# Optimization experiments

Measured on AMD Instinct MI355X. Metric: run time of the kernel, lower is better.

The kernel has to match this reference:

```python
import jax, jax.numpy as jnp
import numpy as np
import math

B, H, S, D = 2, 12, 2048, 64

def setup_inputs() -> dict:
    key = jax.random.key(0)
    kq, kk, kv, km = jax.random.split(key, 4)
    Q = jax.random.normal(kq, (B, H, S, D), dtype=jnp.float32)
    K = jax.random.normal(kk, (B, H, S, D), dtype=jnp.float32)
    V = jax.random.normal(kv, (B, H, S, D), dtype=jnp.float32)
    mask = jax.random.randint(km, (B, 1, S, S), 0, 2, dtype=jnp.int32)
    return {"Q": Q, "K": K, "V": V, "mask": mask}

def reference(Q, K, V, mask):
    d_k = K.shape[-1]
    # [B,H,S,S] scores
    scores = jnp.einsum('bhqd,bhkd->bhqk', Q, K) / math.sqrt(d_k)
    scores = jnp.where(mask == 0, jnp.float32(-1e20), scores)
    attn = jax.nn.softmax(scores, axis=-1)
    # dropout p=0 -> identity
    return jnp.einsum('bhqk,bhkd->bhqd', attn, V)
```

## Files before the change

kernel.cpp:

```cpp
#include <hip/hip_runtime.h>
#include <hip/hip_bf16.h>
#include <math.h>


#define BB 2
#define HH 12
#define SS 2048
#define DD 64
#define BQ 128
#define BK 64
#define GG 4
#define KG (SS / GG)
#define NTG (KG / BK)
#define LT 76
#define NROWS (BB * HH * SS)
#define QSCALE 0.1803368801111f

typedef __attribute__((ext_vector_type(8))) short bf8_t;
typedef __attribute__((ext_vector_type(4))) short bf4_t;
typedef __attribute__((ext_vector_type(4))) float f4_t;
typedef __attribute__((ext_vector_type(4))) unsigned u4_t;
typedef unsigned long long u64;

__device__ __forceinline__ short f2bf(float f) {
    __hip_bfloat16 h = __float2bfloat16(f);
    return *reinterpret_cast<short*>(&h);
}

__device__ __forceinline__ void gl_lds16(const void* g, void* l) {
    __builtin_amdgcn_global_load_lds(
        (const __attribute__((address_space(1))) unsigned*)(g),
        (__attribute__((address_space(3))) unsigned*)(l), 16, 0, 0);
}

__device__ __forceinline__ bf8_t ldfrag(const unsigned short* buf, int row, int c8) {
    return *(const bf8_t*)&buf[((row << 3) | (c8 ^ (row & 7))) << 3];
}

__global__ __launch_bounds__(256) void prepass(
    const float* __restrict__ V, const float* __restrict__ K,
    const int* __restrict__ M, unsigned short* __restrict__ Vt,
    unsigned short* __restrict__ Kb, u64* __restrict__ Mbt)
{
    __shared__ unsigned short Ts[64][LT];
    const int bx   = blockIdx.x;
    const int tid  = threadIdx.x;
    const int w    = tid >> 6;
    const int lane = tid & 63;
    const int b    = bx >> 11;
    const int row  = bx & 2047;

    {
        const int* src = M + (size_t)bx * SS;
        #pragma unroll
        for (int p = 0; p < 8; ++p) {
            int k = p * 256 + w * 64 + lane;
            u64 bm = __ballot(src[k] != 0);
            if (lane == 0)
                Mbt[(size_t)b * 32 * SS + (size_t)(p * 4 + w) * SS + row] = bm;
        }
    }

    if (bx < 768) {
        const int s0 = (bx & 31) * 64;
        const int bh = bx >> 5;
        const float* Vg = V + (size_t)bh * SS * DD;
        #pragma unroll
        for (int pass = 0; pass < 4; ++pass) {
            int c = tid + pass * 256;
            int r = c >> 4, col = (c & 15) * 4;
            float4 v = *(const float4*)(Vg + (size_t)(s0 + r) * DD + col);
            bf4_t p; p.x = f2bf(v.x); p.y = f2bf(v.y); p.z = f2bf(v.z); p.w = f2bf(v.w);
            *(bf4_t*)&Ts[r][col] = p;
        }
        __syncthreads();
        unsigned short* Vo = Vt + (size_t)bh * DD * SS;
        #pragma unroll
        for (int pass = 0; pass < 2; ++pass) {
            int c = tid + pass * 256;
            int d = c >> 3, sc = (c & 7) * 8;
            const int hh32 = sc & 32;
            const int qq4  = (sc >> 1) & 12;
            unsigned short t[8];
            #pragma unroll
            for (int u = 0; u < 4; ++u) t[u]     = Ts[hh32 + qq4 + u][d];
            #pragma unroll
            for (int u = 0; u < 4; ++u) t[4 + u] = Ts[hh32 + 16 + qq4 + u][d];
            uint4 o;
            o.x = (unsigned)t[0] | ((unsigned)t[1] << 16);
            o.y = (unsigned)t[2] | ((unsigned)t[3] << 16);
            o.z = (unsigned)t[4] | ((unsigned)t[5] << 16);
            o.w = (unsigned)t[6] | ((unsigned)t[7] << 16);
            *(uint4*)(Vo + (size_t)d * SS + s0 + sc) = o;
        }
    } else if (bx < 2304) {
        size_t i = ((size_t)(bx - 768) * 256 + tid) * 8;
        float4 a = *(const float4*)(K + i);
        float4 b2 = *(const float4*)(K + i + 4);
        uint4 o;
        o.x = (unsigned short)f2bf(a.x)  | ((unsigned)(unsigned short)f2bf(a.y)  << 16);
        o.y = (unsigned short)f2bf(a.z)  | ((unsigned)(unsigned short)f2bf(a.w)  << 16);
        o.z = (unsigned short)f2bf(b2.x) | ((unsigned)(unsigned short)f2bf(b2.y) << 16);
        o.w = (unsigned short)f2bf(b2.z) | ((unsigned)(unsigned short)f2bf(b2.w) << 16);
        *(uint4*)(Kb + i) = o;
    }
}

__global__ __launch_bounds__(256, 4) void attn_fwd(
    const float* __restrict__ Q, const unsigned short* __restrict__ Kb,
    const unsigned short* __restrict__ Vt, const u64* __restrict__ Mbt,
    float* __restrict__ Opart, float* __restrict__ Lpart)
{
    __shared__ unsigned short Ks[2 * BK * DD];
    __shared__ unsigned short Vts[2 * BK * DD];

    const int tid  = threadIdx.x;
    const int w    = tid >> 6;
    const int lane = tid & 63;
    const int quad = lane >> 4;
    const int l16  = lane & 15;
    const int q0   = blockIdx.x * BQ;
    const int bh   = blockIdx.y;
    const int g    = blockIdx.z;
    const int b    = bh / HH;
    const int qbase = w * 32;

    const float*          Qg = Q  + (size_t)bh * SS * DD;
    const unsigned short* Kg = Kb + (size_t)bh * SS * DD;
    const unsigned short* Vg = Vt + (size_t)bh * DD * SS;
    float* Og = Opart + ((size_t)g * BB * HH + bh) * SS * DD;
    float* Lg = Lpart + (size_t)g * NROWS + (size_t)bh * SS;

    bf8_t bq[2][2];
    #pragma unroll
    for (int qf = 0; qf < 2; ++qf)
        #pragma unroll
        for (int ks = 0; ks < 2; ++ks) {
            const float* qp = Qg + (size_t)(q0 + qbase + qf * 16 + l16) * DD
                                 + ks * 32 + quad * 8;
            float4 x = *(const float4*)qp;
            float4 y = *(const float4*)(qp + 4);
            bf8_t f;
            f[0] = f2bf(x.x * QSCALE); f[1] = f2bf(x.y * QSCALE);
            f[2] = f2bf(x.z * QSCALE); f[3] = f2bf(x.w * QSCALE);
            f[4] = f2bf(y.x * QSCALE); f[5] = f2bf(y.y * QSCALE);
            f[6] = f2bf(y.z * QSCALE); f[7] = f2bf(y.w * QSCALE);
            bq[qf][ks] = f;
        }

    bf8_t onesf;
    {
        short ov = (l16 == 0) ? (short)0x3F80 : (short)0;
        #pragma unroll
        for (int j = 0; j < 8; ++j) onesf[j] = ov;
    }

    f4_t oacc[2][4], lacc[2];
    #pragma unroll
    for (int qf = 0; qf < 2; ++qf) {
        lacc[qf] = (f4_t){0.f, 0.f, 0.f, 0.f};
        #pragma unroll
        for (int nf = 0; nf < 4; ++nf) oacc[qf][nf] = (f4_t){0.f, 0.f, 0.f, 0.f};
    }

    const unsigned short* kSrc[2];
    const unsigned short* vSrc[2];
    unsigned short*       kDst[2];
    unsigned short*       vDst[2];
    #pragma unroll
    for (int j = 0; j < 2; ++j) {
        const int bc = (w * 2 + j) * 64;
        const int c  = bc + lane;
        const int r  = c >> 3;
        const int c8 = (c & 7) ^ (r & 7);
        kSrc[j] = Kg + (size_t)(g * KG + r) * DD + c8 * 8;
        vSrc[j] = Vg + (size_t)r * SS + g * KG + c8 * 8;
        kDst[j] = Ks  + bc * 8;
        vDst[j] = Vts + bc * 8;
    }
    const u64* mp[2];
    u64 mpf[2];
    #pragma unroll
    for (int qf = 0; qf < 2; ++qf) {
        mp[qf] = Mbt + (size_t)b * 32 * SS + (size_t)(g * NTG) * SS
                     + q0 + qbase + qf * 16 + l16;
        mpf[qf] = *mp[qf];
    }

    #pragma unroll
    for (int j = 0; j < 2; ++j) {
        gl_lds16(kSrc[j], kDst[j]);
        gl_lds16(vSrc[j], vDst[j]);
        kSrc[j] += BK * DD;
        vSrc[j] += BK;
    }
    __syncthreads();

    for (int t = 0; t < NTG; ++t) {
        const int cb = (t & 1) * (BK * DD);
        if (t + 1 < NTG) {
            const int nb = ((t + 1) & 1) * (BK * DD);
            #pragma unroll
            for (int j = 0; j < 2; ++j) {
                gl_lds16(kSrc[j], kDst[j] + nb);
                gl_lds16(vSrc[j], vDst[j] + nb);
                kSrc[j] += BK * DD;
                vSrc[j] += BK;
            }
        }
        const u64 cm[2] = {mpf[0] >> (quad * 4), mpf[1] >> (quad * 4)};
        if (t + 1 < NTG) {
            #pragma unroll
            for (int qf = 0; qf < 2; ++qf) {
                mp[qf] += SS;
                mpf[qf] = *mp[qf];
            }
        }
        const unsigned short* Kst = Ks  + cb;
        const unsigned short* Vst = Vts + cb;

        #pragma unroll
        for (int h = 0; h < 2; ++h) {
            unsigned aw[2][4];
            #pragma unroll
            for (int kfh = 0; kfh < 2; ++kfh) {
                const int kf = h * 2 + kfh;
                bf8_t ak0 = ldfrag(Kst, kf * 16 + l16, quad);
                bf8_t ak1 = ldfrag(Kst, kf * 16 + l16, 4 + quad);
                #pragma unroll
                for (int qf = 0; qf < 2; ++qf) {
                    f4_t s = (f4_t){0.f, 0.f, 0.f, 0.f};
                    s = __builtin_amdgcn_mfma_f32_16x16x32_bf16(ak0, bq[qf][0], s, 0, 0, 0);
                    s = __builtin_amdgcn_mfma_f32_16x16x32_bf16(ak1, bq[qf][1], s, 0, 0, 0);
                    float e[4];
                    #pragma unroll
                    for (int r = 0; r < 4; ++r) {
                        float v = __builtin_amdgcn_exp2f(s[r]);
                        e[r] = ((cm[qf] >> (kf * 16 + r)) & 1ull) ? v : 0.f;
                    }
                    aw[qf][kfh * 2 + 0] = __builtin_amdgcn_perm(
                        __float_as_uint(e[1]), __float_as_uint(e[0]), 0x07060302u);
                    aw[qf][kfh * 2 + 1] = __builtin_amdgcn_perm(
                        __float_as_uint(e[3]), __float_as_uint(e[2]), 0x07060302u);
                }
            }
            bf8_t ap[2];
            #pragma unroll
            for (int qf = 0; qf < 2; ++qf) {
                u4_t wds = (u4_t){aw[qf][0], aw[qf][1], aw[qf][2], aw[qf][3]};
                ap[qf] = __builtin_bit_cast(bf8_t, wds);
                lacc[qf] = __builtin_amdgcn_mfma_f32_16x16x32_bf16(
                    ap[qf], onesf, lacc[qf], 0, 0, 0);
            }
            #pragma unroll
            for (int nf = 0; nf < 4; ++nf) {
                bf8_t bv = ldfrag(Vst, nf * 16 + l16, h * 4 + quad);
                #pragma unroll
                for (int qf = 0; qf < 2; ++qf)
                    oacc[qf][nf] = __builtin_amdgcn_mfma_f32_16x16x32_bf16(
                        ap[qf], bv, oacc[qf][nf], 0, 0, 0);
            }
        }
        if (t + 1 < NTG) __syncthreads();
    }

    #pragma unroll
    for (int qf = 0; qf < 2; ++qf) {
        #pragma unroll
        for (int r = 0; r < 4; ++r) {
            const int row = q0 + qbase + qf * 16 + quad * 4 + r;
            #pragma unroll
            for (int nf = 0; nf < 4; ++nf)
                Og[(size_t)row * DD + nf * 16 + l16] = oacc[qf][nf][r];
        }
        if (l16 == 0) {
            #pragma unroll
            for (int r = 0; r < 4; ++r)
                Lg[q0 + qbase + qf * 16 + quad * 4 + r] = lacc[qf][r];
        }
    }
}

__global__ __launch_bounds__(256) void reduce_o(
    const float* __restrict__ Opart, const float* __restrict__ Lpart,
    float* __restrict__ O)
{
    const size_t idx = (size_t)blockIdx.x * 256 + threadIdx.x;
    const size_t row = idx >> 4;
    const int    c   = (int)(idx & 15) * 4;
    float4 acc = {0.f, 0.f, 0.f, 0.f};
    float  l   = 0.f;
    #pragma unroll
    for (int g = 0; g < GG; ++g) {
        float4 a = *(const float4*)(Opart + ((size_t)g * NROWS + row) * DD + c);
        acc.x += a.x; acc.y += a.y; acc.z += a.z; acc.w += a.w;
        l += Lpart[(size_t)g * NROWS + row];
    }
    const float inv = 1.f / l;
    float4 o;
    o.x = acc.x * inv; o.y = acc.y * inv; o.z = acc.z * inv; o.w = acc.w * inv;
    *(float4*)(O + row * DD + c) = o;
}

extern "C" void kernel_launch(void* const* d_in, const int* in_sizes, int n_in,
                              void* d_out, int out_size, void* d_ws, size_t ws_size,
                              hipStream_t stream) {
    const float* Q = (const float*)d_in[0];
    const float* K = (const float*)d_in[1];
    const float* V = (const float*)d_in[2];
    const int*   M = (const int*)d_in[3];
    float*       O = (float*)d_out;

    unsigned short* Vt    = (unsigned short*)d_ws;
    unsigned short* Kb    = Vt + (size_t)BB * HH * SS * DD;
    u64*            Mbt   = (u64*)(Kb + (size_t)BB * HH * SS * DD);
    float*          Opart = (float*)(Mbt + (size_t)BB * 32 * SS);
    float*          Lpart = Opart + (size_t)GG * NROWS * DD;

    prepass<<<dim3(BB * SS), 256, 0, stream>>>(V, K, M, Vt, Kb, Mbt);
    attn_fwd<<<dim3(SS / BQ, BB * HH, GG), 256, 0, stream>>>(Q, Kb, Vt, Mbt,
                                                             Opart, Lpart);
    reduce_o<<<dim3((NROWS * DD / 4) / 256), 256, 0, stream>>>(Opart, Lpart, O);
}
```

Baseline: 157.6 us.

## Double query tile to 256 rows with 512-thread blocks and MFMA priority boost

Each attention block now handles 256 query rows with 8 waves instead of 128 rows with 4, so every staged K/V tile in LDS is shared by twice as many waves, and each thread issues one global-to-LDS copy per tile instead of two. The grid shrinks to half as many blocks. s_setprio is raised around the P·V MFMA section so waves in their matrix phase get scheduling priority over waves doing exp/mask work. The trade-offs are fewer blocks for load balance, heavier barriers across 8 waves, and launch bounds of 512 threads with 4 blocks per unit, which may pressure registers.

```diff
diff --git a/kernel.cpp b/kernel.cpp
--- a/kernel.cpp
+++ b/kernel.cpp
@@ -7,11 +7,12 @@
 #define HH 12
 #define SS 2048
 #define DD 64
-#define BQ 128
+#define BQ 256
 #define BK 64
 #define GG 4
 #define KG (SS / GG)
 #define NTG (KG / BK)
+#define NQB (SS / BQ)
 #define LT 76
 #define NROWS (BB * HH * SS)
 #define QSCALE 0.1803368801111f
@@ -106,7 +107,7 @@
     }
 }
 
-__global__ __launch_bounds__(256, 4) void attn_fwd(
+__global__ __launch_bounds__(512, 4) void attn_fwd(
     const float* __restrict__ Q, const unsigned short* __restrict__ Kb,
     const unsigned short* __restrict__ Vt, const u64* __restrict__ Mbt,
     float* __restrict__ Opart, float* __restrict__ Lpart)
@@ -163,20 +164,19 @@
         for (int nf = 0; nf < 4; ++nf) oacc[qf][nf] = (f4_t){0.f, 0.f, 0.f, 0.f};
     }
 
-    const unsigned short* kSrc[2];
-    const unsigned short* vSrc[2];
-    unsigned short*       kDst[2];
-    unsigned short*       vDst[2];
-    #pragma unroll
-    for (int j = 0; j < 2; ++j) {
-        const int bc = (w * 2 + j) * 64;
+    const unsigned short* kSrc;
+    const unsigned short* vSrc;
+    unsigned short*       kDst;
+    unsigned short*       vDst;
+    {
+        const int bc = w * 64;
         const int c  = bc + lane;
         const int r  = c >> 3;
         const int c8 = (c & 7) ^ (r & 7);
-        kSrc[j] = Kg + (size_t)(g * KG + r) * DD + c8 * 8;
-        vSrc[j] = Vg + (size_t)r * SS + g * KG + c8 * 8;
-        kDst[j] = Ks  + bc * 8;
-        vDst[j] = Vts + bc * 8;
+        kSrc = Kg + (size_t)(g * KG + r) * DD + c8 * 8;
+        vSrc = Vg + (size_t)r * SS + g * KG + c8 * 8;
+        kDst = Ks  + bc * 8;
+        vDst = Vts + bc * 8;
     }
     const u64* mp[2];
     u64 mpf[2];
@@ -187,26 +187,20 @@
         mpf[qf] = *mp[qf];
     }
 
-    #pragma unroll
-    for (int j = 0; j < 2; ++j) {
-        gl_lds16(kSrc[j], kDst[j]);
-        gl_lds16(vSrc[j], vDst[j]);
-        kSrc[j] += BK * DD;
-        vSrc[j] += BK;
-    }
+    gl_lds16(kSrc, kDst);
+    gl_lds16(vSrc, vDst);
+    kSrc += BK * DD;
+    vSrc += BK;
     __syncthreads();
 
     for (int t = 0; t < NTG; ++t) {
         const int cb = (t & 1) * (BK * DD);
         if (t + 1 < NTG) {
             const int nb = ((t + 1) & 1) * (BK * DD);
-            #pragma unroll
-            for (int j = 0; j < 2; ++j) {
-                gl_lds16(kSrc[j], kDst[j] + nb);
-                gl_lds16(vSrc[j], vDst[j] + nb);
-                kSrc[j] += BK * DD;
-                vSrc[j] += BK;
-            }
+            gl_lds16(kSrc, kDst + nb);
+            gl_lds16(vSrc, vDst + nb);
+            kSrc += BK * DD;
+            vSrc += BK;
         }
         const u64 cm[2] = {mpf[0] >> (quad * 4), mpf[1] >> (quad * 4)};
         if (t + 1 < NTG) {
@@ -245,6 +239,7 @@
                 }
             }
             bf8_t ap[2];
+            __builtin_amdgcn_s_setprio(1);
             #pragma unroll
             for (int qf = 0; qf < 2; ++qf) {
                 u4_t wds = (u4_t){aw[qf][0], aw[qf][1], aw[qf][2], aw[qf][3]};
@@ -260,6 +255,7 @@
                     oacc[qf][nf] = __builtin_amdgcn_mfma_f32_16x16x32_bf16(
                         ap[qf], bv, oacc[qf][nf], 0, 0, 0);
             }
+            __builtin_amdgcn_s_setprio(0);
         }
         if (t + 1 < NTG) __syncthreads();
     }
@@ -318,7 +314,7 @@
     float*          Lpart = Opart + (size_t)GG * NROWS * DD;
 
     prepass<<<dim3(BB * SS), 256, 0, stream>>>(V, K, M, Vt, Kb, Mbt);
-    attn_fwd<<<dim3(SS / BQ, BB * HH, GG), 256, 0, stream>>>(Q, Kb, Vt, Mbt,
-                                                             Opart, Lpart);
+    attn_fwd<<<dim3(NQB, BB * HH, GG), 512, 0, stream>>>(Q, Kb, Vt, Mbt,
+                                                         Opart, Lpart);
     reduce_o<<<dim3((NROWS * DD / 4) / 256), 256, 0, stream>>>(Opart, Lpart, O);
 }
```

New measurement: 157.7 us. Within noise of the previous version (+0.1%).
